# Optimization experiments

Hardware: AMD Instinct MI355X
Metric: run time of the kernel (lower is better)

## Reference

```python
import jax, jax.numpy as jnp
import numpy as np

WIN = 8
NUM_HEADS = 4
DIM = 128


def _relative_position_index(ws):
    coords = np.stack(np.meshgrid(np.arange(ws), np.arange(ws), indexing='ij'))  # (2, ws, ws)
    cf = coords.reshape(2, -1)                      # (2, ws*ws)
    rel = (cf[:, :, None] - cf[:, None, :]).transpose(1, 2, 0).astype(np.int64)  # (N, N, 2)
    rel[..., 0] += ws - 1
    rel[..., 1] += ws - 1
    rel[..., 0] *= 2 * ws - 1
    return rel.sum(-1)                              # (N, N) int64


def setup_inputs() -> dict:
    key = jax.random.key(0)
    ks = jax.random.split(key, 8)
    B_, N, C = 4096, WIN * WIN, DIM
    nW = 4096
    x = jax.random.normal(ks[0], (B_, N, C), dtype=jnp.float32)
    mask = jax.random.normal(ks[1], (nW, N, N), dtype=jnp.float32)
    wq = jax.random.normal(ks[2], (C, C), dtype=jnp.float32) * 0.02
    bq = jnp.zeros((C,), dtype=jnp.float32)
    wkv = jax.random.normal(ks[3], (2 * C, C), dtype=jnp.float32) * 0.02
    bkv = jnp.zeros((2 * C,), dtype=jnp.float32)
    bias_table = jax.random.normal(ks[4], ((2 * WIN - 1) * (2 * WIN - 1), NUM_HEADS), dtype=jnp.float32) * 0.02
    wproj = jax.random.normal(ks[5], (C, C), dtype=jnp.float32) * 0.02
    bproj = jnp.zeros((C,), dtype=jnp.float32)
    rel_index = jnp.asarray(_relative_position_index(WIN))
    return {"x": x, "wq": wq, "bq": bq, "wkv": wkv, "bkv": bkv,
            "bias_table": bias_table, "wproj": wproj, "bproj": bproj,
            "mask": mask, "rel_index": rel_index}


def reference(x, wq, bq, wkv, bkv, bias_table, wproj, bproj, mask, rel_index):
    B_, N, C = x.shape
    H = NUM_HEADS
    d = C // H
    scale = d ** -0.5
    # qkv projection (attn_kv=None path)
    q = (x @ wq.T + bq).reshape(B_, N, H, d).transpose(0, 2, 1, 3)      # (B_, H, N, d)
    kv = (x @ wkv.T + bkv).reshape(B_, N, 2, H, d)
    k = kv[:, :, 0].transpose(0, 2, 1, 3)                               # (B_, H, N, d)
    v = kv[:, :, 1].transpose(0, 2, 1, 3)
    attn = jnp.einsum('bhnd,bhmd->bhnm', q * scale, k)                  # (B_, H, N, N)
    # relative position bias gather: (N*N,) -> (N, N, H) -> (H, N, N)
    rpb = bias_table[rel_index.reshape(-1)].reshape(N, N, H).transpose(2, 0, 1)
    attn = attn + rpb[None]
    # shifted-window mask: attn viewed as (B_//nW, nW, H, N, N) + mask (nW, 1, N, N)
    nW = mask.shape[0]
    attn = (attn.reshape(B_ // nW, nW, H, N, N) + mask[None, :, None]).reshape(B_, H, N, N)
    attn = jax.nn.softmax(attn, axis=-1)
    out = jnp.einsum('bhnm,bhmd->bhnd', attn, v).transpose(0, 2, 1, 3).reshape(B_, N, C)
    return out @ wproj.T + bproj
```

## Files before the change

kernel.cpp:

```cpp
#include <hip/hip_runtime.h>


typedef __bf16 bf16x8 __attribute__((ext_vector_type(8)));
typedef __bf16 bf16x4 __attribute__((ext_vector_type(4)));
typedef float f32x4 __attribute__((ext_vector_type(4)));

#define LOG2E 1.4426950408889634f
#define QSCALE (0.17677669529663687f * 1.4426950408889634f)

__global__ __launch_bounds__(256)
void prep_kernel(const float* __restrict__ wq,
                 const float* __restrict__ wkv,
                 const float* __restrict__ wp,
                 const float* __restrict__ bt,
                 const int* __restrict__ ri,
                 char* __restrict__ ws) {
  int t = blockIdx.x * 256 + (int)threadIdx.x;
  if (t < 8192) {
    int s = t >> 11;
    int c = t & 2047;
    int lane = c & 63, kk = (c >> 6) & 3, ct = c >> 8;
    int li = lane & 15, q4 = lane >> 4;
    int col = ct * 16 + li;
    int ko = kk * 32 + q4 * 8;
    const float* src = (s == 0) ? (wq + col * 128 + ko)
                     : (s == 1) ? (wkv + col * 128 + ko)
                     : (s == 2) ? (wkv + (col + 128) * 128 + ko)
                                : (wp + col * 128 + ko);
    bf16x8 v;
#pragma unroll
    for (int i = 0; i < 8; ++i) v[i] = (__bf16)src[i];
    *(bf16x8*)(ws + s * 32768 + c * 16) = v;
  } else {
    int c = t - 8192;
    int lane = c & 63, tj = (c >> 6) & 3, ti = (c >> 8) & 3, h = (c >> 10) & 3;
    int li = lane & 15, q4 = lane >> 4;
    int qt = tj * 16 + li;
    f32x4 r;
#pragma unroll
    for (int rr = 0; rr < 4; ++rr) {
      int kt = ti * 16 + q4 * 4 + rr;
      r[rr] = LOG2E * bt[ri[qt * 64 + kt] * 4 + h];
    }
    *(f32x4*)(ws + 131072 + c * 16) = r;
  }
}

static __device__ __forceinline__ bf16x8 cvt8(const float* __restrict__ p) {
  f32x4 a = *(const f32x4*)p;
  f32x4 b = *((const f32x4*)p + 1);
  bf16x8 r;
#pragma unroll
  for (int i = 0; i < 4; ++i) { r[i] = (__bf16)a[i]; r[i + 4] = (__bf16)b[i]; }
  return r;
}

static __device__ __forceinline__ int xaddr(int r, int c) {
  return (r << 8) + ((((c >> 3) ^ (r & 7)) << 4)) + ((c & 7) << 1);
}
static __device__ __forceinline__ int qaddr(int r, int c) {
  return (r << 6) + ((((c >> 3) ^ ((r >> 2) & 3)) << 4)) + ((c & 7) << 1);
}
static __device__ __forceinline__ int paddr(int r, int c) {
  return (r << 7) + ((((c >> 3) ^ (r & 7)) << 4)) + ((c & 7) << 1);
}
static __device__ __forceinline__ int vtaddr(int dd, int m) {
  return (dd << 7) + ((((m >> 3) ^ (dd & 7)) << 4)) + ((m & 7) << 1);
}

#define MFMA16(acc, afr, bfr) \
  acc = __builtin_amdgcn_mfma_f32_16x16x32_bf16(afr, bfr, acc, 0, 0, 0)

__global__ __launch_bounds__(256, 2)
void winattn_kernel(const float* __restrict__ xg,
                    const float* __restrict__ bq,
                    const float* __restrict__ bkv,
                    const float* __restrict__ bp,
                    const float* __restrict__ mask,
                    const char* __restrict__ ws,
                    float* __restrict__ out) {
  __shared__ char smem[65536];
  const int b = blockIdx.x;
  const int tid = (int)threadIdx.x;
  const int h = tid >> 6;
  const int lane = tid & 63;
  const int q4 = lane >> 4;
  const int li = lane & 15;
  const int Wb = 16384 + h * 12288;
  const int Qb = Wb, Kb = Wb + 4096, Vb = Wb + 8192, Pb = Wb;
  const bf16x8* __restrict__ wqP = (const bf16x8*)(ws);
  const bf16x8* __restrict__ wkP = (const bf16x8*)(ws + 32768);
  const bf16x8* __restrict__ wvP = (const bf16x8*)(ws + 65536);
  const bf16x8* __restrict__ wpP = (const bf16x8*)(ws + 98304);
  const f32x4* __restrict__ rpbP = (const f32x4*)(ws + 131072);

  {
    const float* xw = xg + (size_t)b * 8192;
#pragma unroll
    for (int rep = 0; rep < 4; ++rep) {
      int chunk = rep * 256 + tid;
      int r = chunk >> 4, cc = chunk & 15;
      bf16x8 v = cvt8(xw + r * 128 + cc * 8);
      *(bf16x8*)(smem + xaddr(r, cc * 8)) = v;
    }
  }
  __syncthreads();

  {
    f32x4 aqT[2][4] = {}; f32x4 akT[2][4] = {}; f32x4 av[4][2] = {};
#pragma unroll
    for (int kk = 0; kk < 4; ++kk) {
      bf16x8 a[4];
#pragma unroll
      for (int nt = 0; nt < 4; ++nt)
        a[nt] = *(const bf16x8*)(smem + xaddr(nt * 16 + li, kk * 32 + q4 * 8));
#pragma unroll
      for (int mt = 0; mt < 2; ++mt) {
        int wi = ((h * 2 + mt) * 4 + kk) * 64 + lane;
        bf16x8 wbq = wqP[wi];
        bf16x8 wbk = wkP[wi];
        bf16x8 wbv = wvP[wi];
#pragma unroll
        for (int nt = 0; nt < 4; ++nt) {
          MFMA16(aqT[mt][nt], wbq, a[nt]);
          MFMA16(akT[mt][nt], wbk, a[nt]);
          MFMA16(av[nt][mt], a[nt], wbv);
        }
      }
    }
#pragma unroll
    for (int mt = 0; mt < 2; ++mt) {
      f32x4 bq4 = *(const f32x4*)(bq + h * 32 + mt * 16 + q4 * 4);
      f32x4 bk4 = *(const f32x4*)(bkv + h * 32 + mt * 16 + q4 * 4);
      int f0 = mt * 16 + q4 * 4;
#pragma unroll
      for (int nt = 0; nt < 4; ++nt) {
        bf16x4 qv, kv;
#pragma unroll
        for (int rr = 0; rr < 4; ++rr) {
          qv[rr] = (__bf16)((aqT[mt][nt][rr] + bq4[rr]) * QSCALE);
          kv[rr] = (__bf16)(akT[mt][nt][rr] + bk4[rr]);
        }
        int row = nt * 16 + li;
        *(bf16x4*)(smem + Qb + qaddr(row, f0)) = qv;
        *(bf16x4*)(smem + Kb + qaddr(row, f0)) = kv;
      }
    }
#pragma unroll
    for (int tj = 0; tj < 2; ++tj) {
      float bvv = bkv[h * 32 + tj * 16 + li + 128];
      int lc = tj * 16 + li;
#pragma unroll
      for (int ti = 0; ti < 4; ++ti) {
        bf16x4 vv;
#pragma unroll
        for (int rr = 0; rr < 4; ++rr) vv[rr] = (__bf16)(av[ti][tj][rr] + bvv);
        *(bf16x4*)(smem + Vb + vtaddr(lc, ti * 16 + q4 * 4)) = vv;
      }
    }
  }

  f32x4 bias[4][4];
  {
    const float* mw = mask + (size_t)b * 4096;
#pragma unroll
    for (int ti = 0; ti < 4; ++ti)
#pragma unroll
      for (int tj = 0; tj < 4; ++tj) {
        f32x4 rv = rpbP[((h * 4 + ti) * 4 + tj) * 64 + lane];
        f32x4 mv = *(const f32x4*)(mw + (tj * 16 + li) * 64 + ti * 16 + q4 * 4);
#pragma unroll
        for (int rr = 0; rr < 4; ++rr) rv[rr] = fmaf(LOG2E, mv[rr], rv[rr]);
        bias[ti][tj] = rv;
      }
  }
  asm volatile("s_waitcnt lgkmcnt(0)" ::: "memory");

  f32x4 S[4][4];
  {
    bf16x8 qf[4], kf[4];
#pragma unroll
    for (int t = 0; t < 4; ++t) {
      qf[t] = *(const bf16x8*)(smem + Qb + qaddr(t * 16 + li, q4 * 8));
      kf[t] = *(const bf16x8*)(smem + Kb + qaddr(t * 16 + li, q4 * 8));
    }
#pragma unroll
    for (int ti = 0; ti < 4; ++ti)
#pragma unroll
      for (int tj = 0; tj < 4; ++tj)
        S[ti][tj] = __builtin_amdgcn_mfma_f32_16x16x32_bf16(
            kf[ti], qf[tj], bias[ti][tj], 0, 0, 0);
  }

#pragma unroll
  for (int tj = 0; tj < 4; ++tj) {
    float mx = S[0][tj][0];
#pragma unroll
    for (int ti = 0; ti < 4; ++ti)
#pragma unroll
      for (int rr = 0; rr < 4; ++rr) mx = fmaxf(mx, S[ti][tj][rr]);
    mx = fmaxf(mx, __shfl_xor(mx, 16));
    mx = fmaxf(mx, __shfl_xor(mx, 32));
    float s = 0.f;
#pragma unroll
    for (int ti = 0; ti < 4; ++ti)
#pragma unroll
      for (int rr = 0; rr < 4; ++rr) {
        float e = __builtin_amdgcn_exp2f(S[ti][tj][rr] - mx);
        S[ti][tj][rr] = e;
        s += e;
      }
    s += __shfl_xor(s, 16);
    s += __shfl_xor(s, 32);
    float rinv = __builtin_amdgcn_rcpf(s);
#pragma unroll
    for (int ti = 0; ti < 4; ++ti)
#pragma unroll
      for (int rr = 0; rr < 4; ++rr) S[ti][tj][rr] *= rinv;
  }

#pragma unroll
  for (int ti = 0; ti < 4; ++ti)
#pragma unroll
    for (int tj = 0; tj < 4; ++tj) {
      bf16x4 pv;
#pragma unroll
      for (int rr = 0; rr < 4; ++rr) pv[rr] = (__bf16)S[ti][tj][rr];
      *(bf16x4*)(smem + Pb + paddr(tj * 16 + li, ti * 16 + q4 * 4)) = pv;
    }
  asm volatile("s_waitcnt lgkmcnt(0)" ::: "memory");

  f32x4 OT[2][4] = {};
#pragma unroll
  for (int ks = 0; ks < 2; ++ks) {
    bf16x8 pf[4], vf[2];
#pragma unroll
    for (int nt = 0; nt < 4; ++nt)
      pf[nt] = *(const bf16x8*)(smem + Pb + paddr(nt * 16 + li, ks * 32 + q4 * 8));
#pragma unroll
    for (int mt = 0; mt < 2; ++mt)
      vf[mt] = *(const bf16x8*)(smem + Vb + vtaddr(mt * 16 + li, ks * 32 + q4 * 8));
#pragma unroll
    for (int mt = 0; mt < 2; ++mt)
#pragma unroll
      for (int nt = 0; nt < 4; ++nt)
        MFMA16(OT[mt][nt], vf[mt], pf[nt]);
  }

  __syncthreads();
#pragma unroll
  for (int mt = 0; mt < 2; ++mt) {
    int f0 = h * 32 + mt * 16 + q4 * 4;
#pragma unroll
    for (int nt = 0; nt < 4; ++nt) {
      bf16x4 yv;
#pragma unroll
      for (int rr = 0; rr < 4; ++rr) yv[rr] = (__bf16)OT[mt][nt][rr];
      *(bf16x4*)(smem + xaddr(nt * 16 + li, f0)) = yv;
    }
  }
  __syncthreads();

  {
    f32x4 acc[2][4] = {};
#pragma unroll
    for (int kk = 0; kk < 4; ++kk) {
      bf16x8 a[4];
#pragma unroll
      for (int nt = 0; nt < 4; ++nt)
        a[nt] = *(const bf16x8*)(smem + xaddr(nt * 16 + li, kk * 32 + q4 * 8));
#pragma unroll
      for (int mt = 0; mt < 2; ++mt) {
        int wi = ((h * 2 + mt) * 4 + kk) * 64 + lane;
        bf16x8 wb = wpP[wi];
#pragma unroll
        for (int nt = 0; nt < 4; ++nt)
          MFMA16(acc[mt][nt], wb, a[nt]);
      }
    }
    float* ow = out + (size_t)b * 8192;
#pragma unroll
    for (int mt = 0; mt < 2; ++mt) {
      f32x4 bp4 = *(const f32x4*)(bp + h * 32 + mt * 16 + q4 * 4);
#pragma unroll
      for (int nt = 0; nt < 4; ++nt) {
        f32x4 o;
#pragma unroll
        for (int rr = 0; rr < 4; ++rr) o[rr] = acc[mt][nt][rr] + bp4[rr];
        *(f32x4*)(ow + (nt * 16 + li) * 128 + h * 32 + mt * 16 + q4 * 4) = o;
      }
    }
  }
}

extern "C" void kernel_launch(void* const* d_in, const int* in_sizes, int n_in,
                              void* d_out, int out_size, void* d_ws, size_t ws_size,
                              hipStream_t stream) {
  (void)in_sizes; (void)n_in; (void)ws_size; (void)out_size;
  prep_kernel<<<96, 256, 0, stream>>>(
      (const float*)d_in[1],
      (const float*)d_in[3],
      (const float*)d_in[6],
      (const float*)d_in[5],
      (const int*)d_in[9],
      (char*)d_ws);
  winattn_kernel<<<4096, 256, 0, stream>>>(
      (const float*)d_in[0],
      (const float*)d_in[2],
      (const float*)d_in[4],
      (const float*)d_in[7],
      (const float*)d_in[8],
      (const char*)d_ws,
      (float*)d_out);
}
```

Before: 326.7 us.

## Split each head across two waves with 512-thread blocks

```diff
diff --git a/kernel.cpp b/kernel.cpp
--- a/kernel.cpp
+++ b/kernel.cpp
@@ -71,7 +71,7 @@
 #define MFMA16(acc, afr, bfr) \
   acc = __builtin_amdgcn_mfma_f32_16x16x32_bf16(afr, bfr, acc, 0, 0, 0)
 
-__global__ __launch_bounds__(256, 2)
+__global__ __launch_bounds__(512, 4)
 void winattn_kernel(const float* __restrict__ xg,
                     const float* __restrict__ bq,
                     const float* __restrict__ bkv,
@@ -82,7 +82,9 @@
   __shared__ char smem[65536];
   const int b = blockIdx.x;
   const int tid = (int)threadIdx.x;
-  const int h = tid >> 6;
+  const int wid = tid >> 6;
+  const int h = wid >> 1;
+  const int half = wid & 1;
   const int lane = tid & 63;
   const int q4 = lane >> 4;
   const int li = lane & 15;
@@ -97,8 +99,8 @@
   {
     const float* xw = xg + (size_t)b * 8192;
 #pragma unroll
-    for (int rep = 0; rep < 4; ++rep) {
-      int chunk = rep * 256 + tid;
+    for (int rep = 0; rep < 2; ++rep) {
+      int chunk = rep * 512 + tid;
       int r = chunk >> 4, cc = chunk & 15;
       bf16x8 v = cvt8(xw + r * 128 + cc * 8);
       *(bf16x8*)(smem + xaddr(r, cc * 8)) = v;
@@ -107,13 +109,14 @@
   __syncthreads();
 
   {
-    f32x4 aqT[2][4] = {}; f32x4 akT[2][4] = {}; f32x4 av[4][2] = {};
+    f32x4 aqT[2][2] = {}; f32x4 akT[2][2] = {}; f32x4 av[2][2] = {};
 #pragma unroll
     for (int kk = 0; kk < 4; ++kk) {
-      bf16x8 a[4];
-#pragma unroll
-      for (int nt = 0; nt < 4; ++nt)
-        a[nt] = *(const bf16x8*)(smem + xaddr(nt * 16 + li, kk * 32 + q4 * 8));
+      bf16x8 a[2];
+#pragma unroll
+      for (int ntl = 0; ntl < 2; ++ntl)
+        a[ntl] = *(const bf16x8*)(smem +
+                   xaddr((half * 2 + ntl) * 16 + li, kk * 32 + q4 * 8));
 #pragma unroll
       for (int mt = 0; mt < 2; ++mt) {
         int wi = ((h * 2 + mt) * 4 + kk) * 64 + lane;
@@ -121,10 +124,10 @@
         bf16x8 wbk = wkP[wi];
         bf16x8 wbv = wvP[wi];
 #pragma unroll
-        for (int nt = 0; nt < 4; ++nt) {
-          MFMA16(aqT[mt][nt], wbq, a[nt]);
-          MFMA16(akT[mt][nt], wbk, a[nt]);
-          MFMA16(av[nt][mt], a[nt], wbv);
+        for (int ntl = 0; ntl < 2; ++ntl) {
+          MFMA16(aqT[mt][ntl], wbq, a[ntl]);
+          MFMA16(akT[mt][ntl], wbk, a[ntl]);
+          MFMA16(av[ntl][mt], a[ntl], wbv);
         }
       }
     }
@@ -134,71 +137,74 @@
       f32x4 bk4 = *(const f32x4*)(bkv + h * 32 + mt * 16 + q4 * 4);
       int f0 = mt * 16 + q4 * 4;
 #pragma unroll
-      for (int nt = 0; nt < 4; ++nt) {
+      for (int ntl = 0; ntl < 2; ++ntl) {
         bf16x4 qv, kv;
 #pragma unroll
         for (int rr = 0; rr < 4; ++rr) {
-          qv[rr] = (__bf16)((aqT[mt][nt][rr] + bq4[rr]) * QSCALE);
-          kv[rr] = (__bf16)(akT[mt][nt][rr] + bk4[rr]);
+          qv[rr] = (__bf16)((aqT[mt][ntl][rr] + bq4[rr]) * QSCALE);
+          kv[rr] = (__bf16)(akT[mt][ntl][rr] + bk4[rr]);
         }
-        int row = nt * 16 + li;
+        int row = (half * 2 + ntl) * 16 + li;
         *(bf16x4*)(smem + Qb + qaddr(row, f0)) = qv;
         *(bf16x4*)(smem + Kb + qaddr(row, f0)) = kv;
       }
     }
 #pragma unroll
-    for (int tj = 0; tj < 2; ++tj) {
-      float bvv = bkv[h * 32 + tj * 16 + li + 128];
-      int lc = tj * 16 + li;
-#pragma unroll
-      for (int ti = 0; ti < 4; ++ti) {
+    for (int mt = 0; mt < 2; ++mt) {
+      float bvv = bkv[h * 32 + mt * 16 + li + 128];
+      int lc = mt * 16 + li;
+#pragma unroll
+      for (int ntl = 0; ntl < 2; ++ntl) {
         bf16x4 vv;
 #pragma unroll
-        for (int rr = 0; rr < 4; ++rr) vv[rr] = (__bf16)(av[ti][tj][rr] + bvv);
-        *(bf16x4*)(smem + Vb + vtaddr(lc, ti * 16 + q4 * 4)) = vv;
-      }
-    }
-  }
-
-  f32x4 bias[4][4];
+        for (int rr = 0; rr < 4; ++rr) vv[rr] = (__bf16)(av[ntl][mt][rr] + bvv);
+        *(bf16x4*)(smem + Vb + vtaddr(lc, (half * 2 + ntl) * 16 + q4 * 4)) = vv;
+      }
+    }
+  }
+
+  f32x4 bias[4][2];
   {
     const float* mw = mask + (size_t)b * 4096;
 #pragma unroll
     for (int ti = 0; ti < 4; ++ti)
 #pragma unroll
-      for (int tj = 0; tj < 4; ++tj) {
+      for (int tjl = 0; tjl < 2; ++tjl) {
+        int tj = half * 2 + tjl;
         f32x4 rv = rpbP[((h * 4 + ti) * 4 + tj) * 64 + lane];
         f32x4 mv = *(const f32x4*)(mw + (tj * 16 + li) * 64 + ti * 16 + q4 * 4);
 #pragma unroll
         for (int rr = 0; rr < 4; ++rr) rv[rr] = fmaf(LOG2E, mv[rr], rv[rr]);
-        bias[ti][tj] = rv;
-      }
-  }
-  asm volatile("s_waitcnt lgkmcnt(0)" ::: "memory");
-
-  f32x4 S[4][4];
-  {
-    bf16x8 qf[4], kf[4];
-#pragma unroll
-    for (int t = 0; t < 4; ++t) {
-      qf[t] = *(const bf16x8*)(smem + Qb + qaddr(t * 16 + li, q4 * 8));
-      kf[t] = *(const bf16x8*)(smem + Kb + qaddr(t * 16 + li, q4 * 8));
-    }
-#pragma unroll
-    for (int ti = 0; ti < 4; ++ti)
-#pragma unroll
-      for (int tj = 0; tj < 4; ++tj)
-        S[ti][tj] = __builtin_amdgcn_mfma_f32_16x16x32_bf16(
-            kf[ti], qf[tj], bias[ti][tj], 0, 0, 0);
-  }
-
-#pragma unroll
-  for (int tj = 0; tj < 4; ++tj) {
-    float mx = S[0][tj][0];
-#pragma unroll
-    for (int ti = 0; ti < 4; ++ti)
-#pragma unroll
-      for (int rr = 0; rr < 4; ++rr) mx = fmaxf(mx, S[ti][tj][rr]);
+        bias[ti][tjl] = rv;
+      }
+  }
+  __syncthreads();
+
+  f32x4 S[4][2];
+  {
+    bf16x8 qf[2], kf[4];
+#pragma unroll
+    for (int tjl = 0; tjl < 2; ++tjl)
+      qf[tjl] = *(const bf16x8*)(smem +
+                  Qb + qaddr((half * 2 + tjl) * 16 + li, q4 * 8));
+#pragma unroll
+    for (int ti = 0; ti < 4; ++ti)
+      kf[ti] = *(const bf16x8*)(smem + Kb + qaddr(ti * 16 + li, q4 * 8));
+#pragma unroll
+    for (int ti = 0; ti < 4; ++ti)
+#pragma unroll
+      for (int tjl = 0; tjl < 2; ++tjl)
+        S[ti][tjl] = __builtin_amdgcn_mfma_f32_16x16x32_bf16(
+            kf[ti], qf[tjl], bias[ti][tjl], 0, 0, 0);
+  }
+
+#pragma unroll
+  for (int tjl = 0; tjl < 2; ++tjl) {
+    float mx = S[0][tjl][0];
+#pragma unroll
+    for (int ti = 0; ti < 4; ++ti)
+#pragma unroll
+      for (int rr = 0; rr < 4; ++rr) mx = fmaxf(mx, S[ti][tjl][rr]);
     mx = fmaxf(mx, __shfl_xor(mx, 16));
     mx = fmaxf(mx, __shfl_xor(mx, 32));
     float s = 0.f;
@@ -206,8 +212,8 @@
     for (int ti = 0; ti < 4; ++ti)
 #pragma unroll
       for (int rr = 0; rr < 4; ++rr) {
-        float e = __builtin_amdgcn_exp2f(S[ti][tj][rr] - mx);
-        S[ti][tj][rr] = e;
+        float e = __builtin_amdgcn_exp2f(S[ti][tjl][rr] - mx);
+        S[ti][tjl][rr] = e;
         s += e;
       }
     s += __shfl_xor(s, 16);
@@ -216,66 +222,70 @@
 #pragma unroll
     for (int ti = 0; ti < 4; ++ti)
 #pragma unroll
-      for (int rr = 0; rr < 4; ++rr) S[ti][tj][rr] *= rinv;
-  }
+      for (int rr = 0; rr < 4; ++rr) S[ti][tjl][rr] *= rinv;
+  }
+  __syncthreads();
 
 #pragma unroll
   for (int ti = 0; ti < 4; ++ti)
 #pragma unroll
-    for (int tj = 0; tj < 4; ++tj) {
+    for (int tjl = 0; tjl < 2; ++tjl) {
       bf16x4 pv;
 #pragma unroll
-      for (int rr = 0; rr < 4; ++rr) pv[rr] = (__bf16)S[ti][tj][rr];
-      *(bf16x4*)(smem + Pb + paddr(tj * 16 + li, ti * 16 + q4 * 4)) = pv;
+      for (int rr = 0; rr < 4; ++rr) pv[rr] = (__bf16)S[ti][tjl][rr];
+      *(bf16x4*)(smem + Pb +
+                 paddr((half * 2 + tjl) * 16 + li, ti * 16 + q4 * 4)) = pv;
     }
   asm volatile("s_waitcnt lgkmcnt(0)" ::: "memory");
 
-  f32x4 OT[2][4] = {};
+  f32x4 OT[2][2] = {};
 #pragma unroll
   for (int ks = 0; ks < 2; ++ks) {
-    bf16x8 pf[4], vf[2];
-#pragma unroll
-    for (int nt = 0; nt < 4; ++nt)
-      pf[nt] = *(const bf16x8*)(smem + Pb + paddr(nt * 16 + li, ks * 32 + q4 * 8));
+    bf16x8 pf[2], vf[2];
+#pragma unroll
+    for (int ntl = 0; ntl < 2; ++ntl)
+      pf[ntl] = *(const bf16x8*)(smem + Pb +
+                  paddr((half * 2 + ntl) * 16 + li, ks * 32 + q4 * 8));
 #pragma unroll
     for (int mt = 0; mt < 2; ++mt)
-      vf[mt] = *(const bf16x8*)(smem + Vb + vtaddr(mt * 16 + li, ks * 32 + q4 * 8));
+      vf[mt] = *(const bf16x8*)(smem + Vb +
+                  vtaddr(mt * 16 + li, ks * 32 + q4 * 8));
 #pragma unroll
     for (int mt = 0; mt < 2; ++mt)
 #pragma unroll
-      for (int nt = 0; nt < 4; ++nt)
-        MFMA16(OT[mt][nt], vf[mt], pf[nt]);
-  }
-
-  __syncthreads();
+      for (int ntl = 0; ntl < 2; ++ntl)
+        MFMA16(OT[mt][ntl], vf[mt], pf[ntl]);
+  }
+
 #pragma unroll
   for (int mt = 0; mt < 2; ++mt) {
     int f0 = h * 32 + mt * 16 + q4 * 4;
 #pragma unroll
-    for (int nt = 0; nt < 4; ++nt) {
+    for (int ntl = 0; ntl < 2; ++ntl) {
       bf16x4 yv;
 #pragma unroll
-      for (int rr = 0; rr < 4; ++rr) yv[rr] = (__bf16)OT[mt][nt][rr];
-      *(bf16x4*)(smem + xaddr(nt * 16 + li, f0)) = yv;
+      for (int rr = 0; rr < 4; ++rr) yv[rr] = (__bf16)OT[mt][ntl][rr];
+      *(bf16x4*)(smem + xaddr((half * 2 + ntl) * 16 + li, f0)) = yv;
     }
   }
   __syncthreads();
 
   {
-    f32x4 acc[2][4] = {};
+    f32x4 acc[2][2] = {};
 #pragma unroll
     for (int kk = 0; kk < 4; ++kk) {
-      bf16x8 a[4];
-#pragma unroll
-      for (int nt = 0; nt < 4; ++nt)
-        a[nt] = *(const bf16x8*)(smem + xaddr(nt * 16 + li, kk * 32 + q4 * 8));
+      bf16x8 a[2];
+#pragma unroll
+      for (int ntl = 0; ntl < 2; ++ntl)
+        a[ntl] = *(const bf16x8*)(smem +
+                   xaddr((half * 2 + ntl) * 16 + li, kk * 32 + q4 * 8));
 #pragma unroll
       for (int mt = 0; mt < 2; ++mt) {
         int wi = ((h * 2 + mt) * 4 + kk) * 64 + lane;
         bf16x8 wb = wpP[wi];
 #pragma unroll
-        for (int nt = 0; nt < 4; ++nt)
-          MFMA16(acc[mt][nt], wb, a[nt]);
+        for (int ntl = 0; ntl < 2; ++ntl)
+          MFMA16(acc[mt][ntl], wb, a[ntl]);
       }
     }
     float* ow = out + (size_t)b * 8192;
@@ -283,11 +293,12 @@
     for (int mt = 0; mt < 2; ++mt) {
       f32x4 bp4 = *(const f32x4*)(bp + h * 32 + mt * 16 + q4 * 4);
 #pragma unroll
-      for (int nt = 0; nt < 4; ++nt) {
+      for (int ntl = 0; ntl < 2; ++ntl) {
         f32x4 o;
 #pragma unroll
-        for (int rr = 0; rr < 4; ++rr) o[rr] = acc[mt][nt][rr] + bp4[rr];
-        *(f32x4*)(ow + (nt * 16 + li) * 128 + h * 32 + mt * 16 + q4 * 4) = o;
+        for (int rr = 0; rr < 4; ++rr) o[rr] = acc[mt][ntl][rr] + bp4[rr];
+        *(f32x4*)(ow + ((half * 2 + ntl) * 16 + li) * 128 +
+                  h * 32 + mt * 16 + q4 * 4) = o;
       }
     }
   }
@@ -304,7 +315,7 @@
       (const float*)d_in[5],
       (const int*)d_in[9],
       (char*)d_ws);
-  winattn_kernel<<<4096, 256, 0, stream>>>(
+  winattn_kernel<<<4096, 512, 0, stream>>>(
       (const float*)d_in[0],
       (const float*)d_in[2],
       (const float*)d_in[4],
```

Result: slower. 342.3 us (+4.8%).
